# Kernel optimization log

Measured on AMD Instinct MI355X. Metric: run time of the kernel, lower is better.

Reference implementation:

```python
import jax, jax.numpy as jnp
import numpy as np

ON_OFF = "off"  # init kwarg: 'off' includes the next-frame temporal candidate

def setup_inputs() -> dict:
    key = jax.random.key(0)
    k1, k2 = jax.random.split(key)
    xs = jax.random.normal(k1, (4, 32, 128, 32), dtype=jnp.float32)  # [B,T,N,D]
    A = jax.random.randint(k2, (1, 128, 128), 0, 2, dtype=jnp.int32)  # [1,N,N] adjacency
    return {"xs": xs, "A": A}

def reference(xs, A):
    B, T, N, D = xs.shape
    # A_f = A + I ; neighbors are nonzero entries (self-loop included via eye)
    A_f = A[0].astype(xs.dtype) + jnp.eye(N, dtype=xs.dtype)
    spatial_mask = A_f != 0  # [N,N] : spatial_mask[n, j] -> j is neighbor of n

    # Candidate set per (frame t, node n): prev-frame self, next-frame self (on_off=='off'),
    # and all spatial neighbors at frame t. Padded to fixed size K = N + 2 with masks.
    spat = jnp.broadcast_to(xs[:, :, None, :, :], (B, T, N, N, D))   # [B,T,N,N,D]
    prev = jnp.concatenate([xs[:, :1], xs[:, :-1]], axis=1)          # [B,T,N,D] (t=0 masked)
    nxt = jnp.concatenate([xs[:, 1:], xs[:, -1:]], axis=1)           # [B,T,N,D] (t=T-1 masked)
    cand = jnp.concatenate([prev[:, :, :, None, :], nxt[:, :, :, None, :], spat], axis=3)  # [B,T,N,N+2,D]

    t = jnp.arange(T)
    prev_m = jnp.broadcast_to((t > 0)[:, None, None], (T, N, 1))
    if ON_OFF == "off":
        next_m = jnp.broadcast_to((t < T - 1)[:, None, None], (T, N, 1))
    else:
        next_m = jnp.zeros((T, N, 1), dtype=bool)
    sp_m = jnp.broadcast_to(spatial_mask[None], (T, N, N))
    mask = jnp.concatenate([prev_m, next_m, sp_m], axis=2)  # [T,N,N+2]

    # Masked median = torch.median semantics (lower median): sort with +inf padding,
    # pick index (k-1)//2 where k = number of valid candidates.
    vals = jnp.where(mask[None, :, :, :, None], cand, jnp.inf)
    vals = jnp.sort(vals, axis=3)
    k = mask.sum(axis=2)              # [T,N]
    med_idx = (k - 1) // 2            # lower median index
    idx = jnp.broadcast_to(med_idx[None, :, :, None, None], (B, T, N, 1, D))
    ys = jnp.take_along_axis(vals, idx, axis=3)[:, :, :, 0, :]  # [B,T,N,D]
    return ys
```

## Files before the change

kernel.cpp:

```cpp
#include <hip/hip_runtime.h>
#include <stdint.h>
#include <math.h>

#define BB 4
#define TT 32
#define NN 128
#define DD 32
#define NPB 16
#define TPB (NPB * DD)
#define NBLK (BB * TT * (NN / NPB))
#define CAP 16
#define SSTR (TPB + 4)

#define SID_PREV 0xFEu
#define SID_NEXT 0xFFu

__device__ __forceinline__ int bin8(float x) {
    int i = (int)fmaf(x, 5.0f, 4.0f);
    i = i < 0 ? 0 : i;
    return i > 7 ? 7 : i;
}

__global__ __launch_bounds__(TPB) void median_kernel(const float* __restrict__ xs,
                                                     const int* __restrict__ A,
                                                     float* __restrict__ out) {
    __shared__ float sval[NN * DD];
    __shared__ uint8_t sbin[NN * DD];
    __shared__ __align__(16) uint32_t sbit[8 * DD * 4];
    __shared__ uint32_t snbr_w[NPB * NN / 4];
    __shared__ __align__(16) uint32_t smask[NPB][4];
    __shared__ int sdeg[NPB];
    __shared__ uint8_t slist[(CAP + 1) * SSTR];

    const int tid = threadIdx.x;
    const int bid = blockIdx.x;
    const int g = ((bid & 7) << 7) | (bid >> 3);
    const int ng = g & (NN / NPB - 1);
    const int t  = (g >> 3) & (TT - 1);
    const int b  = g >> 8;
    const int n0 = ng * NPB;

    const int d = tid & (DD - 1);
    const int nl = tid >> 5;
    const int n = n0 + nl;
    const int pv = (t > 0) ? 1 : 0;
    const int nv = (t < TT - 1) ? 1 : 0;
    const int ne = pv + nv;

    float exv0 = 0.0f, exv1 = 0.0f;
    if (pv) exv0 = xs[(((size_t)(b * TT + t - 1) * NN) + n) * DD + d];
    if (nv) {
        float v = xs[(((size_t)(b * TT + t + 1) * NN) + n) * DD + d];
        if (pv) exv1 = v; else exv0 = v;
    }

    const float4* src4 = (const float4*)(xs + ((size_t)(b * TT + t) * NN) * DD);
    #pragma unroll
    for (int s = 0; s < 2; ++s) {
        int i4 = tid + (s << 9);
        float4 f = src4[i4];
        ((float4*)sval)[i4] = f;
        uint32_t pk = (uint32_t)bin8(f.x) | ((uint32_t)bin8(f.y) << 8)
                    | ((uint32_t)bin8(f.z) << 16) | ((uint32_t)bin8(f.w) << 24);
        ((uint32_t*)sbin)[i4] = pk;
    }

    {
        uint8_t* snbr = (uint8_t*)snbr_w;
        const int lane = tid & 63;
        const int wid = tid >> 6;
        const unsigned long long lmask = (1ULL << lane) - 1ULL;
        #pragma unroll
        for (int h = 0; h < 2; ++h) {
            const int rr = wid * 2 + h;
            const int nrow = n0 + rr;
            const int* arow = A + nrow * NN;
            const bool b0 = (arow[lane] != 0) || (lane == nrow);
            const bool b1 = (arow[lane + 64] != 0) || (lane + 64 == nrow);
            const unsigned long long m0 = __ballot(b0);
            const unsigned long long m1 = __ballot(b1);
            const int c0 = __popcll(m0);
            if (b0) snbr[rr * NN + __popcll(m0 & lmask)] = (uint8_t)lane;
            if (b1) snbr[rr * NN + c0 + __popcll(m1 & lmask)] = (uint8_t)(lane + 64);
            if (lane == 0) {
                sdeg[rr] = c0 + __popcll(m1);
                smask[rr][0] = (uint32_t)m0;
                smask[rr][1] = (uint32_t)(m0 >> 32);
                smask[rr][2] = (uint32_t)m1;
                smask[rr][3] = (uint32_t)(m1 >> 32);
            }
        }
    }
    __syncthreads();

    {
        const int rep = tid >> 7;
        const int wo  = (tid >> 5) & 3;
        const int dd  = tid & 31;
        const int ba = rep * 2, bc = ba + 1;
        uint32_t lo = 0u, hi = 0u;
        #pragma unroll 8
        for (int q = 0; q < 32; ++q) {
            const int bv = (int)sbin[(wo * 32 + q) * DD + dd];
            lo |= (bv == ba) ? (1u << q) : 0u;
            hi |= (bv == bc) ? (1u << q) : 0u;
        }
        sbit[ba * 128 + dd * 4 + wo] = lo;
        sbit[bc * 128 + dd * 4 + wo] = hi;
    }
    __syncthreads();

    const int dg = sdeg[nl];
    const int k = dg + ne;
    const uint32_t r = (uint32_t)((k - 1) >> 1);
    const uint8_t* nb = (const uint8_t*)snbr_w + nl * NN;
    const float INFV = __uint_as_float(0x7F800000u);
    const int be0 = bin8(exv0);
    const int be1 = bin8(exv1);

    const uint4 am4 = *((const uint4*)smask[nl]);
    int hist[8];
    const uint4* sbit4 = (const uint4*)sbit;
    #pragma unroll
    for (int bb = 0; bb < 8; ++bb) {
        uint4 w = sbit4[bb * 32 + d];
        hist[bb] = __popc(w.x & am4.x) + __popc(w.y & am4.y)
                 + __popc(w.z & am4.z) + __popc(w.w & am4.w);
    }

    uint32_t cum = 0, lowcnt = 0, mexp = 0;
    int selbin = -1;
    #pragma unroll
    for (int bb = 0; bb < 8; ++bb) {
        uint32_t bc = (uint32_t)hist[bb] + ((ne >= 1 && be0 == bb) ? 1u : 0u)
                                         + ((ne == 2 && be1 == bb) ? 1u : 0u);
        uint32_t nc = cum + bc;
        if (selbin < 0 && r < nc) { selbin = bb; lowcnt = cum; mexp = bc; }
        cum = nc;
    }
    const bool fb = (mexp > CAP);
    const uint32_t rp = r - lowcnt;
    const int storebin = fb ? -1 : selbin;

    const int sb = fb ? 0 : selbin;
    const uint4 wsel = sbit4[sb * 32 + d];
    unsigned long long bm0 = (((unsigned long long)(wsel.y & am4.y)) << 32) | (wsel.x & am4.x);
    unsigned long long bm1 = (((unsigned long long)(wsel.w & am4.w)) << 32) | (wsel.z & am4.z);
    const int mc_sp = fb ? 0 : (__popcll(bm0) + __popcll(bm1));
    #pragma unroll
    for (int u = 0; u < CAP; ++u) {
        const bool lo = (bm0 != 0ull);
        const unsigned long long mm_ = lo ? bm0 : bm1;
        const int ff = __ffsll((unsigned long long)mm_) - 1;
        const uint32_t id = (uint32_t)((lo ? ff : 64 + ff) & 127);
        slist[u * SSTR + tid] = (uint8_t)id;
        const unsigned long long cl = mm_ & (mm_ - 1ull);
        bm0 = lo ? cl : bm0;
        bm1 = lo ? bm1 : cl;
    }
    int mc = mc_sp;
    if (ne >= 1) {
        int slot = mc > CAP ? CAP : mc;
        slist[slot * SSTR + tid] = (uint8_t)SID_PREV;
        mc += (be0 == storebin);
    }
    if (ne == 2) {
        int slot = mc > CAP ? CAP : mc;
        slist[slot * SSTR + tid] = (uint8_t)SID_NEXT;
        mc += (be1 == storebin);
    }

    auto bandval = [&](int e) -> float {
        uint32_t id = slist[e * SSTR + tid];
        float v = sval[(id & 127u) * DD + d];
        v = (id == SID_PREV) ? exv0 : v;
        v = (id == SID_NEXT) ? exv1 : v;
        return v;
    };

    float ki[CAP];
    uint32_t cn[CAP];
    #pragma unroll
    for (int u = 0; u < CAP; ++u) {
        float v = bandval(u);
        ki[u] = (u < mc) ? v : INFV;
        cn[u] = 0;
    }
    int mm = mc;
    #pragma unroll
    for (int off = 32; off; off >>= 1) {
        int o = __shfl_xor(mm, off);
        mm = mm > o ? mm : o;
    }
    {
        int j = 0;
        for (; j + 2 <= mm; j += 2) {
            float x0 = bandval(j);
            float x1 = bandval(j + 1);
            x0 = (j < mc) ? x0 : INFV;
            x1 = (j + 1 < mc) ? x1 : INFV;
            #pragma unroll
            for (int u = 0; u < CAP; ++u) cn[u] += (x0 < ki[u]) + (x1 < ki[u]);
        }
        if (j < mm) {
            float x = bandval(j);
            x = (j < mc) ? x : INFV;
            #pragma unroll
            for (int u = 0; u < CAP; ++u) cn[u] += (x < ki[u]);
        }
    }
    float result = 0.0f;
    bool found = fb;
    #pragma unroll
    for (int u = 0; u < CAP; ++u) {
        if (!found && u < mc && cn[u] == rp) { result = ki[u]; found = true; }
    }

    if (__ballot(!found)) {
        uint32_t eq[CAP];
        #pragma unroll
        for (int u = 0; u < CAP; ++u) eq[u] = 0;
        for (int j = 0; j < mm; ++j) {
            float x = bandval(j);
            x = (j < mc) ? x : INFV;
            #pragma unroll
            for (int u = 0; u < CAP; ++u) eq[u] += (x == ki[u]);
        }
        #pragma unroll
        for (int u = 0; u < CAP; ++u) {
            if (!found && u < mc && cn[u] <= rp && rp < cn[u] + eq[u]) {
                result = ki[u]; found = true;
            }
        }
    }

    if (__ballot(fb)) {
        bool done = !fb;
        for (int i0 = 0; __ballot(!done && i0 < k); i0 += 8) {
            float k8[8]; uint32_t c8[8];
            #pragma unroll
            for (int u = 0; u < 8; ++u) {
                int i = i0 + u;
                float sv = sval[nb[i & 127] * DD + d];
                float ev = ((i - dg) == 0) ? exv0 : exv1;
                float v = (i < dg) ? sv : ev;
                k8[u] = (i < k) ? v : INFV;
                c8[u] = 0;
            }
            for (int j = 0; j < dg; ++j) {
                float xv = sval[nb[j] * DD + d];
                #pragma unroll
                for (int u = 0; u < 8; ++u) c8[u] += (xv < k8[u]);
            }
            if (ne >= 1) {
                #pragma unroll
                for (int u = 0; u < 8; ++u) c8[u] += (exv0 < k8[u]);
            }
            if (ne == 2) {
                #pragma unroll
                for (int u = 0; u < 8; ++u) c8[u] += (exv1 < k8[u]);
            }
            #pragma unroll
            for (int u = 0; u < 8; ++u) {
                if (!done && (i0 + u) < k && c8[u] == r) { result = k8[u]; done = true; }
            }
        }
        if (__ballot(!done)) {
            for (int i0 = 0; __ballot(!done && i0 < k); i0 += 4) {
                float k4[4]; uint32_t lt4[4], le4[4];
                #pragma unroll
                for (int u = 0; u < 4; ++u) {
                    int i = i0 + u;
                    float sv = sval[nb[i & 127] * DD + d];
                    float ev = ((i - dg) == 0) ? exv0 : exv1;
                    float v = (i < dg) ? sv : ev;
                    k4[u] = (i < k) ? v : INFV;
                    lt4[u] = 0; le4[u] = 0;
                }
                for (int j = 0; j < dg; ++j) {
                    float xv = sval[nb[j] * DD + d];
                    #pragma unroll
                    for (int u = 0; u < 4; ++u) { lt4[u] += (xv < k4[u]); le4[u] += (xv <= k4[u]); }
                }
                if (ne >= 1) {
                    #pragma unroll
                    for (int u = 0; u < 4; ++u) { lt4[u] += (exv0 < k4[u]); le4[u] += (exv0 <= k4[u]); }
                }
                if (ne == 2) {
                    #pragma unroll
                    for (int u = 0; u < 4; ++u) { lt4[u] += (exv1 < k4[u]); le4[u] += (exv1 <= k4[u]); }
                }
                #pragma unroll
                for (int u = 0; u < 4; ++u) {
                    if (!done && (i0 + u) < k && lt4[u] <= r && r < le4[u]) {
                        result = k4[u]; done = true;
                    }
                }
            }
        }
    }

    out[(((size_t)(b * TT + t) * NN) + n) * DD + d] = result;
}

extern "C" void kernel_launch(void* const* d_in, const int* in_sizes, int n_in,
                              void* d_out, int out_size, void* d_ws, size_t ws_size,
                              hipStream_t stream) {
    const float* xs = (const float*)d_in[0];
    const int* A = (const int*)d_in[1];
    float* out = (float*)d_out;
    (void)d_ws; (void)ws_size;

    median_kernel<<<NBLK, TPB, 0, stream>>>(xs, A, out);
}
```

Measured before the change: 116.5 us.

## Keep bin candidate list in registers and rank with fixed all-pairs compare

The per-thread candidate IDs for the selected histogram bin are no longer staged in a shared-memory byte list. They are kept in a register array, and their values are loaded directly into registers. The prev/next temporal candidates become two extra fixed slots. Rank counting becomes a fully unrolled 18x18 register compare instead of a wave-max-bounded loop that re-reads shared memory. This removes the shared-memory list and its traffic but adds a fixed quadratic compare cost per thread and more register pressure.

```diff
diff --git a/kernel.cpp b/kernel.cpp
--- a/kernel.cpp
+++ b/kernel.cpp
@@ -10,10 +10,7 @@
 #define TPB (NPB * DD)
 #define NBLK (BB * TT * (NN / NPB))
 #define CAP 16
-#define SSTR (TPB + 4)
-
-#define SID_PREV 0xFEu
-#define SID_NEXT 0xFFu
+#define NK (CAP + 2)
 
 __device__ __forceinline__ int bin8(float x) {
     int i = (int)fmaf(x, 5.0f, 4.0f);
@@ -30,7 +27,6 @@
     __shared__ uint32_t snbr_w[NPB * NN / 4];
     __shared__ __align__(16) uint32_t smask[NPB][4];
     __shared__ int sdeg[NPB];
-    __shared__ uint8_t slist[(CAP + 1) * SSTR];
 
     const int tid = threadIdx.x;
     const int bid = blockIdx.x;
@@ -140,95 +136,55 @@
     }
     const bool fb = (mexp > CAP);
     const uint32_t rp = r - lowcnt;
-    const int storebin = fb ? -1 : selbin;
 
     const int sb = fb ? 0 : selbin;
     const uint4 wsel = sbit4[sb * 32 + d];
     unsigned long long bm0 = (((unsigned long long)(wsel.y & am4.y)) << 32) | (wsel.x & am4.x);
     unsigned long long bm1 = (((unsigned long long)(wsel.w & am4.w)) << 32) | (wsel.z & am4.z);
     const int mc_sp = fb ? 0 : (__popcll(bm0) + __popcll(bm1));
+    int ids[CAP];
     #pragma unroll
     for (int u = 0; u < CAP; ++u) {
         const bool lo = (bm0 != 0ull);
         const unsigned long long mm_ = lo ? bm0 : bm1;
         const int ff = __ffsll((unsigned long long)mm_) - 1;
-        const uint32_t id = (uint32_t)((lo ? ff : 64 + ff) & 127);
-        slist[u * SSTR + tid] = (uint8_t)id;
+        ids[u] = (lo ? ff : 64 + ff) & 127;
         const unsigned long long cl = mm_ & (mm_ - 1ull);
         bm0 = lo ? cl : bm0;
         bm1 = lo ? bm1 : cl;
     }
-    int mc = mc_sp;
-    if (ne >= 1) {
-        int slot = mc > CAP ? CAP : mc;
-        slist[slot * SSTR + tid] = (uint8_t)SID_PREV;
-        mc += (be0 == storebin);
-    }
-    if (ne == 2) {
-        int slot = mc > CAP ? CAP : mc;
-        slist[slot * SSTR + tid] = (uint8_t)SID_NEXT;
-        mc += (be1 == storebin);
-    }
-
-    auto bandval = [&](int e) -> float {
-        uint32_t id = slist[e * SSTR + tid];
-        float v = sval[(id & 127u) * DD + d];
-        v = (id == SID_PREV) ? exv0 : v;
-        v = (id == SID_NEXT) ? exv1 : v;
-        return v;
-    };
-
-    float ki[CAP];
-    uint32_t cn[CAP];
-    #pragma unroll
-    for (int u = 0; u < CAP; ++u) {
-        float v = bandval(u);
-        ki[u] = (u < mc) ? v : INFV;
-        cn[u] = 0;
-    }
-    int mm = mc;
-    #pragma unroll
-    for (int off = 32; off; off >>= 1) {
-        int o = __shfl_xor(mm, off);
-        mm = mm > o ? mm : o;
-    }
-    {
-        int j = 0;
-        for (; j + 2 <= mm; j += 2) {
-            float x0 = bandval(j);
-            float x1 = bandval(j + 1);
-            x0 = (j < mc) ? x0 : INFV;
-            x1 = (j + 1 < mc) ? x1 : INFV;
-            #pragma unroll
-            for (int u = 0; u < CAP; ++u) cn[u] += (x0 < ki[u]) + (x1 < ki[u]);
-        }
-        if (j < mm) {
-            float x = bandval(j);
-            x = (j < mc) ? x : INFV;
-            #pragma unroll
-            for (int u = 0; u < CAP; ++u) cn[u] += (x < ki[u]);
-        }
-    }
+
+    float ki[NK];
+    #pragma unroll
+    for (int u = 0; u < CAP; ++u)
+        ki[u] = (u < mc_sp) ? sval[ids[u] * DD + d] : INFV;
+    const bool t0 = (ne >= 1) && (be0 == selbin) && !fb;
+    const bool t1 = (ne == 2) && (be1 == selbin) && !fb;
+    ki[CAP]     = t0 ? exv0 : INFV;
+    ki[CAP + 1] = t1 ? exv1 : INFV;
+
     float result = 0.0f;
     bool found = fb;
     #pragma unroll
-    for (int u = 0; u < CAP; ++u) {
-        if (!found && u < mc && cn[u] == rp) { result = ki[u]; found = true; }
+    for (int u = 0; u < NK; ++u) {
+        uint32_t cnu = 0;
+        #pragma unroll
+        for (int v = 0; v < NK; ++v) cnu += (ki[v] < ki[u]) ? 1u : 0u;
+        const bool valid = (u < CAP) ? (u < mc_sp) : ((u == CAP) ? t0 : t1);
+        if (!found && valid && cnu == rp) { result = ki[u]; found = true; }
     }
 
     if (__ballot(!found)) {
-        uint32_t eq[CAP];
         #pragma unroll
-        for (int u = 0; u < CAP; ++u) eq[u] = 0;
-        for (int j = 0; j < mm; ++j) {
-            float x = bandval(j);
-            x = (j < mc) ? x : INFV;
+        for (int u = 0; u < NK; ++u) {
+            uint32_t cnu = 0, equ = 0;
             #pragma unroll
-            for (int u = 0; u < CAP; ++u) eq[u] += (x == ki[u]);
-        }
-        #pragma unroll
-        for (int u = 0; u < CAP; ++u) {
-            if (!found && u < mc && cn[u] <= rp && rp < cn[u] + eq[u]) {
+            for (int v = 0; v < NK; ++v) {
+                cnu += (ki[v] < ki[u]) ? 1u : 0u;
+                equ += (ki[v] == ki[u]) ? 1u : 0u;
+            }
+            const bool valid = (u < CAP) ? (u < mc_sp) : ((u == CAP) ? t0 : t1);
+            if (!found && valid && cnu <= rp && rp < cnu + equ) {
                 result = ki[u]; found = true;
             }
         }
```

Result: faster. 110.1 us (-5.5%).
